# Performance work log

Hardware: AMD Instinct MI355X
Metric: run time of the kernel (lower is better)

The kernel has to match this reference:

```python
import jax, jax.numpy as jnp
import numpy as np

N_NODES = 100000
N_IN = 256
N_OUT = 64
N_EDGES = 1600000


def setup_inputs() -> dict:
    key = jax.random.key(0)
    k_x, k_w, k_b, k_v, k_r, k_c = jax.random.split(key, 6)
    x = jax.random.normal(k_x, (N_NODES, N_IN), dtype=jnp.float32)
    W = jax.random.normal(k_w, (N_IN, N_OUT), dtype=jnp.float32) * (1.0 / np.sqrt(N_IN))
    b = jax.random.normal(k_b, (N_OUT,), dtype=jnp.float32) * 0.01
    adj_vals = jax.random.uniform(k_v, (N_EDGES,), dtype=jnp.float32)
    edge_rows = jax.random.randint(k_r, (N_EDGES,), 0, N_NODES, dtype=jnp.int32)
    edge_cols = jax.random.randint(k_c, (N_EDGES,), 0, N_NODES, dtype=jnp.int32)
    return {"x": x, "W": W, "b": b, "adj_vals": adj_vals,
            "edge_rows": edge_rows, "edge_cols": edge_cols}


def reference(x, W, b, adj_vals, edge_rows, edge_cols):
    # linear projection: [N, n_in] @ [n_in, n_out] + b -> [N, n_out]
    h = x @ W + b
    # sparse-dense matmul: out[i] = sum_e adj_vals[e] * h[edge_cols[e]] for edge_rows[e]==i
    msgs = h[edge_cols] * adj_vals[:, None]  # [E, n_out]
    out = jax.ops.segment_sum(msgs, edge_rows, num_segments=N_NODES)
    return out
```

## Files before the change

kernel.cpp:

```cpp
#include <hip/hip_runtime.h>


#include <stdint.h>

constexpr int KDIM = 256;
constexpr int MOUT = 64;

constexpr int RPB = 128;
constexpr int RPB_SHIFT = 7;
constexpr int MAXBUCK = 1024;
constexpr int CHUNK = 2048;
constexpr int COL_BITS = 20;
constexpr int COL_MASK = (1 << COL_BITS) - 1;
constexpr int SORT_CAP = 4096;
constexpr int HIST_BLOCKS = 256;
constexpr int GROWS = 64;

typedef __attribute__((ext_vector_type(8))) short short8v;
typedef __attribute__((ext_vector_type(4))) float f32x4;

__device__ __forceinline__ unsigned short f2bf(float f) {
  unsigned u = __float_as_uint(f);
  return (unsigned short)((u + 0x7fffu + ((u >> 16) & 1u)) >> 16);
}

__device__ __forceinline__ void async_ld16(const float* g, float* l) {
  __builtin_amdgcn_global_load_lds(
      (const __attribute__((address_space(1))) void*)g,
      (__attribute__((address_space(3))) void*)l, 16, 0, 0);
}

__global__ __launch_bounds__(256)
void prep(const float* __restrict__ W, unsigned short* __restrict__ wt,
          const int* __restrict__ rows, int* __restrict__ bcnt, int E, int nbuck) {
  const int t = threadIdx.x;
  if ((int)blockIdx.x < 64) {
    int n = blockIdx.x;
    wt[n * KDIM + t] = f2bf(W[(size_t)t * MOUT + n]);
    return;
  }
  __shared__ int cnt[MAXBUCK];
  for (int i = t; i < nbuck; i += 256) cnt[i] = 0;
  __syncthreads();
  const int b0 = blockIdx.x - 64;
  for (int e = b0 * 256 + t; e < E; e += HIST_BLOCKS * 256)
    atomicAdd(&cnt[rows[e] >> RPB_SHIFT], 1);
  __syncthreads();
  for (int i = t; i < nbuck; i += 256)
    if (cnt[i]) atomicAdd(&bcnt[i], cnt[i]);
}

__global__ __launch_bounds__(1024)
void scan_buckets(const int* __restrict__ bcnt, int* __restrict__ bptr,
                  int* __restrict__ bcur, int nbuck, int E) {
  __shared__ int buf[1024];
  __shared__ int carry;
  const int t = threadIdx.x;
  if (t == 0) carry = 0;
  __syncthreads();
  for (int c0 = 0; c0 < nbuck; c0 += 1024) {
    int i = c0 + t;
    int x = (i < nbuck) ? bcnt[i] : 0;
    buf[t] = x;
    __syncthreads();
    for (int off = 1; off < 1024; off <<= 1) {
      int v = (t >= off) ? buf[t - off] : 0;
      __syncthreads();
      buf[t] += v;
      __syncthreads();
    }
    int incl = buf[t];
    int base = carry;
    if (i < nbuck) {
      int ex = base + incl - x;
      bptr[i] = ex;
      bcur[i] = ex;
    }
    __syncthreads();
    if (t == 1023) carry = base + incl;
    __syncthreads();
  }
  if (t == 0) bptr[nbuck] = E;
}

__global__ __launch_bounds__(256, 4)
void gemm_scatter(const float* __restrict__ x, const unsigned short* __restrict__ wt,
                  const float* __restrict__ bvec, unsigned short* __restrict__ h,
                  const int* __restrict__ rows, const int* __restrict__ cols,
                  const float* __restrict__ vals, int* __restrict__ bcur,
                  int2* __restrict__ sorted, int gemmBlocks, int N, int E, int nbuck) {
  __shared__ __align__(16) char smem[16384];
  const int t = threadIdx.x;

  if ((int)blockIdx.x < gemmBlocks) {
    auto xs = reinterpret_cast<float(*)[GROWS][32]>(smem);
    const int wave = t >> 6, lane = t & 63;
    const int lo = lane & 15, hi = lane >> 4;
    const int row0 = blockIdx.x * GROWS;
    const int rowbase = row0 + wave * 16;

    auto stage = [&](int kt, int b) {
#pragma unroll
      for (int i = 0; i < 2; ++i) {
        int g = i * 256 + t;
        int row = g >> 3, c = g & 7;
        int csw = c ^ (row & 7);
        int rr = row0 + row; if (rr >= N) rr = N - 1;
        const float* src = &x[(size_t)rr * KDIM + kt * 32 + csw * 4];
        float* dst = &xs[b][0][0] + (size_t)(i * 256 + (t & 192)) * 4;
        async_ld16(src, dst);
      }
    };

    float bias[4];
#pragma unroll
    for (int nt = 0; nt < 4; ++nt) bias[nt] = bvec[nt * 16 + lo];

    const int lr = wave * 16 + lo;
    const int go0 = (((hi * 2)    ) ^ (lr & 7)) * 4;
    const int go1 = (((hi * 2) + 1) ^ (lr & 7)) * 4;

    f32x4 acc[4] = {};
    short8v wfr[2][4];
#pragma unroll
    for (int nt = 0; nt < 4; ++nt)
      wfr[0][nt] = *reinterpret_cast<const short8v*>(&wt[(size_t)(nt * 16 + lo) * KDIM + hi * 8]);
    stage(0, 0);

#pragma unroll
    for (int kt = 0; kt < 8; ++kt) {
      const int cb = kt & 1;
      __syncthreads();
      if (kt < 7) {
        stage(kt + 1, cb ^ 1);
#pragma unroll
        for (int nt = 0; nt < 4; ++nt)
          wfr[cb ^ 1][nt] = *reinterpret_cast<const short8v*>(
              &wt[(size_t)(nt * 16 + lo) * KDIM + (kt + 1) * 32 + hi * 8]);
      }
      float4 p0 = *reinterpret_cast<const float4*>(&xs[cb][lr][go0]);
      float4 p1 = *reinterpret_cast<const float4*>(&xs[cb][lr][go1]);
      short8v a;
      a[0] = (short)f2bf(p0.x); a[1] = (short)f2bf(p0.y);
      a[2] = (short)f2bf(p0.z); a[3] = (short)f2bf(p0.w);
      a[4] = (short)f2bf(p1.x); a[5] = (short)f2bf(p1.y);
      a[6] = (short)f2bf(p1.z); a[7] = (short)f2bf(p1.w);
#pragma unroll
      for (int nt = 0; nt < 4; ++nt)
        acc[nt] = __builtin_amdgcn_mfma_f32_16x16x32_bf16(a, wfr[cb][nt], acc[nt], 0, 0, 0);
    }

#pragma unroll
    for (int reg = 0; reg < 4; ++reg) {
      int row = rowbase + hi * 4 + reg;
      if (row < N) {
#pragma unroll
        for (int nt = 0; nt < 4; ++nt)
          h[(size_t)row * MOUT + nt * 16 + lo] = f2bf(acc[nt][reg] + bias[nt]);
      }
    }
    return;
  }

  int* lcnt  = reinterpret_cast<int*>(smem);
  int* lbase = lcnt + MAXBUCK;
  const int cid = blockIdx.x - gemmBlocks;
  const int e0 = cid * CHUNK;
  const int e1 = min(e0 + CHUNK, E);

  for (int i = t; i < nbuck; i += 256) lcnt[i] = 0;
  __syncthreads();
  for (int e = e0 + t; e < e1; e += 256)
    atomicAdd(&lcnt[rows[e] >> RPB_SHIFT], 1);
  __syncthreads();
  for (int i = t; i < nbuck; i += 256) {
    int c = lcnt[i];
    lbase[i] = c ? atomicAdd(&bcur[i], c) : 0;
  }
  __syncthreads();
  for (int i = t; i < nbuck; i += 256) lcnt[i] = 0;
  __syncthreads();
  for (int e = e0 + t; e < e1; e += 256) {
    int r = rows[e];
    int b = r >> RPB_SHIFT;
    int lrow = r & (RPB - 1);
    int pos = lbase[b] + atomicAdd(&lcnt[b], 1);
    sorted[pos] = make_int2((lrow << COL_BITS) | cols[e], __float_as_int(vals[e]));
  }
}

__global__ __launch_bounds__(256)
void bucket_sort(int2* __restrict__ sorted, const int* __restrict__ bptr,
                 int* __restrict__ row_ptr, int* __restrict__ bflag,
                 int N, int E, int nbuck) {
  __shared__ int2 eds[SORT_CAP];
  __shared__ int lcnt[RPB];
  __shared__ int loff[RPB];
  __shared__ int lcur[RPB];
  const int t = threadIdx.x;
  const int b = blockIdx.x;
  const int s = bptr[b];
  const int e = bptr[b + 1];
  const int cnt = e - s;
  const int row0 = b << RPB_SHIFT;

  if (b == 0 && t == 0) row_ptr[N] = E;

  if (cnt > SORT_CAP) {
    if (t == 0) bflag[b] = 1;
    if (t < RPB && row0 + t < N) row_ptr[row0 + t] = s;
    return;
  }
  if (t == 0) bflag[b] = 0;

  if (t < RPB) lcnt[t] = 0;
  __syncthreads();
  for (int j = s + t; j < e; j += 256) {
    int2 p = sorted[j];
    eds[j - s] = p;
    atomicAdd(&lcnt[p.x >> COL_BITS], 1);
  }
  __syncthreads();
  if (t < RPB) loff[t] = lcnt[t];
  __syncthreads();
  for (int off = 1; off < RPB; off <<= 1) {
    int v = (t < RPB && t >= off) ? loff[t - off] : 0;
    __syncthreads();
    if (t < RPB) loff[t] += v;
    __syncthreads();
  }
  if (t < RPB) {
    int ex = loff[t] - lcnt[t];
    loff[t] = ex;
    lcur[t] = 0;
    int grow = row0 + t;
    if (grow < N) row_ptr[grow] = s + ex;
  }
  __syncthreads();
  for (int idx = t; idx < cnt; idx += 256) {
    int2 p = eds[idx];
    int lr = p.x >> COL_BITS;
    int pos = s + loff[lr] + atomicAdd(&lcur[lr], 1);
    sorted[pos] = p;
  }
}

__device__ __forceinline__ void edge_fma(float* acc, const unsigned short* h,
                                         int2 p, int part) {
  float v = __int_as_float(p.y);
  int col = p.x & COL_MASK;
  uint4 hv = *reinterpret_cast<const uint4*>(&h[(size_t)col * MOUT + part * 8]);
  acc[0] += v * __uint_as_float(hv.x << 16);
  acc[1] += v * __uint_as_float(hv.x & 0xffff0000u);
  acc[2] += v * __uint_as_float(hv.y << 16);
  acc[3] += v * __uint_as_float(hv.y & 0xffff0000u);
  acc[4] += v * __uint_as_float(hv.z << 16);
  acc[5] += v * __uint_as_float(hv.z & 0xffff0000u);
  acc[6] += v * __uint_as_float(hv.w << 16);
  acc[7] += v * __uint_as_float(hv.w & 0xffff0000u);
}

__global__ __launch_bounds__(256)
void reduce_rows(const unsigned short* __restrict__ h, const int2* __restrict__ sorted,
                 const int* __restrict__ row_ptr, const int* __restrict__ bptr,
                 const int* __restrict__ bflag, float* __restrict__ out, int N) {
  int row = (blockIdx.x * 256 + threadIdx.x) >> 6;
  if (row >= N) return;
  int lane = threadIdx.x & 63;
  int slot = lane >> 3;
  int part = lane & 7;
  int b = row >> RPB_SHIFT;
  int lrow = row & (RPB - 1);
  bool filt = bflag[b] != 0;

  float acc[8];
#pragma unroll
  for (int i = 0; i < 8; ++i) acc[i] = 0.f;

  if (!filt) {
    int s = row_ptr[row];
    int e = row_ptr[row + 1];
    int j = s + slot;
    for (; j + 8 < e; j += 16) {
      int2 p0 = sorted[j];
      int2 p1 = sorted[j + 8];
      float v0 = __int_as_float(p0.y);
      float v1 = __int_as_float(p1.y);
      uint4 h0 = *reinterpret_cast<const uint4*>(
          &h[(size_t)(p0.x & COL_MASK) * MOUT + part * 8]);
      uint4 h1 = *reinterpret_cast<const uint4*>(
          &h[(size_t)(p1.x & COL_MASK) * MOUT + part * 8]);
      acc[0] += v0 * __uint_as_float(h0.x << 16);
      acc[1] += v0 * __uint_as_float(h0.x & 0xffff0000u);
      acc[2] += v0 * __uint_as_float(h0.y << 16);
      acc[3] += v0 * __uint_as_float(h0.y & 0xffff0000u);
      acc[4] += v0 * __uint_as_float(h0.z << 16);
      acc[5] += v0 * __uint_as_float(h0.z & 0xffff0000u);
      acc[6] += v0 * __uint_as_float(h0.w << 16);
      acc[7] += v0 * __uint_as_float(h0.w & 0xffff0000u);
      acc[0] += v1 * __uint_as_float(h1.x << 16);
      acc[1] += v1 * __uint_as_float(h1.x & 0xffff0000u);
      acc[2] += v1 * __uint_as_float(h1.y << 16);
      acc[3] += v1 * __uint_as_float(h1.y & 0xffff0000u);
      acc[4] += v1 * __uint_as_float(h1.z << 16);
      acc[5] += v1 * __uint_as_float(h1.z & 0xffff0000u);
      acc[6] += v1 * __uint_as_float(h1.w << 16);
      acc[7] += v1 * __uint_as_float(h1.w & 0xffff0000u);
    }
    if (j < e) edge_fma(acc, h, sorted[j], part);
  } else {
    int s = bptr[b];
    int e = bptr[b + 1];
    for (int j = s + slot; j < e; j += 8) {
      int2 p = sorted[j];
      if ((p.x >> COL_BITS) != lrow) continue;
      edge_fma(acc, h, p, part);
    }
  }

#pragma unroll
  for (int m = 8; m <= 32; m <<= 1)
#pragma unroll
    for (int i = 0; i < 8; ++i)
      acc[i] += __shfl_xor(acc[i], m, 64);

  if (slot == 0) {
    float* op = &out[(size_t)row * MOUT + part * 8];
    *reinterpret_cast<float4*>(op)     = make_float4(acc[0], acc[1], acc[2], acc[3]);
    *reinterpret_cast<float4*>(op + 4) = make_float4(acc[4], acc[5], acc[6], acc[7]);
  }
}

__global__ __launch_bounds__(256)
void scatter_edges(const unsigned short* __restrict__ h, const float* __restrict__ vals,
                   const int* __restrict__ rows, const int* __restrict__ cols,
                   float* __restrict__ out, int E) {
  long long idx = (long long)blockIdx.x * blockDim.x + threadIdx.x;
  int e = (int)(idx >> 4);
  int part = (int)(idx & 15);
  if (e >= E) return;
  int r = rows[e];
  int c = cols[e];
  float v = vals[e];
  uint2 hv = *reinterpret_cast<const uint2*>(&h[(size_t)c * MOUT + part * 4]);
  float* op = &out[(size_t)r * MOUT + part * 4];
  atomicAdd(op + 0, v * __uint_as_float(hv.x << 16));
  atomicAdd(op + 1, v * __uint_as_float(hv.x & 0xffff0000u));
  atomicAdd(op + 2, v * __uint_as_float(hv.y << 16));
  atomicAdd(op + 3, v * __uint_as_float(hv.y & 0xffff0000u));
}

__global__ __launch_bounds__(256)
void wt_transpose(const float* __restrict__ W, unsigned short* __restrict__ wt) {
  int n = blockIdx.x;
  int k = threadIdx.x;
  wt[n * KDIM + k] = f2bf(W[(size_t)k * MOUT + n]);
}

static inline size_t align256(size_t x) { return (x + 255) & ~(size_t)255; }

extern "C" void kernel_launch(void* const* d_in, const int* in_sizes, int n_in,
                              void* d_out, int out_size, void* d_ws, size_t ws_size,
                              hipStream_t stream) {
  const float* x    = (const float*)d_in[0];
  const float* W    = (const float*)d_in[1];
  const float* bvec = (const float*)d_in[2];
  const float* vals = (const float*)d_in[3];
  const int* erows  = (const int*)d_in[4];
  const int* ecols  = (const int*)d_in[5];
  float* out = (float*)d_out;

  const int N = in_sizes[0] / KDIM;
  const int E = in_sizes[3];
  const int nbuck = (N + RPB - 1) / RPB;

  char* ws = (char*)d_ws;
  size_t off_h  = 0;
  size_t off_wt = align256(off_h + (size_t)N * MOUT * sizeof(short));
  size_t off_bp = align256(off_wt + (size_t)MOUT * KDIM * sizeof(short));
  size_t off_bc = align256(off_bp + (size_t)(nbuck + 1) * sizeof(int));
  size_t off_cu = align256(off_bc + (size_t)nbuck * sizeof(int));
  size_t off_bf = align256(off_cu + (size_t)nbuck * sizeof(int));
  size_t off_rp = align256(off_bf + (size_t)nbuck * sizeof(int));
  size_t off_sp = align256(off_rp + (size_t)(N + 1) * sizeof(int));
  size_t need   = off_sp + (size_t)E * sizeof(int2);

  unsigned short* h  = (unsigned short*)(ws + off_h);
  unsigned short* wt = (unsigned short*)(ws + off_wt);

  dim3 blk256(256);
  const int gemmBlocks = (N + GROWS - 1) / GROWS;

  if (ws_size >= need && nbuck <= MAXBUCK && N < (1 << COL_BITS)) {
    int* bptr  = (int*)(ws + off_bp);
    int* bcnt  = (int*)(ws + off_bc);
    int* bcur  = (int*)(ws + off_cu);
    int* bflag = (int*)(ws + off_bf);
    int* row_ptr = (int*)(ws + off_rp);
    int2* sorted = (int2*)(ws + off_sp);

    hipMemsetAsync(bcnt, 0, (size_t)nbuck * sizeof(int), stream);
    prep<<<dim3(64 + HIST_BLOCKS), blk256, 0, stream>>>(W, wt, erows, bcnt, E, nbuck);
    scan_buckets<<<dim3(1), dim3(1024), 0, stream>>>(bcnt, bptr, bcur, nbuck, E);
    const int scatBlocks = (E + CHUNK - 1) / CHUNK;
    gemm_scatter<<<dim3(gemmBlocks + scatBlocks), blk256, 0, stream>>>(
        x, wt, bvec, h, erows, ecols, vals, bcur, sorted, gemmBlocks, N, E, nbuck);
    bucket_sort<<<dim3(nbuck), blk256, 0, stream>>>(sorted, bptr, row_ptr, bflag, N, E, nbuck);
    reduce_rows<<<dim3(((size_t)N * 64 + 255) / 256), blk256, 0, stream>>>(
        h, sorted, row_ptr, bptr, bflag, out, N);
  } else {
    wt_transpose<<<dim3(MOUT), blk256, 0, stream>>>(W, wt);
    gemm_scatter<<<dim3(gemmBlocks), blk256, 0, stream>>>(
        x, wt, bvec, h, erows, ecols, vals, (int*)wt, (int2*)h, gemmBlocks, N, E, nbuck);
    hipMemsetAsync(d_out, 0, (size_t)out_size * sizeof(float), stream);
    long long work = (long long)E * 16;
    scatter_edges<<<dim3((unsigned)((work + 255) / 256)), blk256, 0, stream>>>(h, vals, erows, ecols, out, E);
  }
}
```

Baseline: 139.3 us.

## Split fused GEMM/scatter kernel and deepen GEMM K-tile to 64

Measured after the change: 144.5 us. 1.04x slower.

```diff
diff --git a/kernel.cpp b/kernel.cpp
--- a/kernel.cpp
+++ b/kernel.cpp
@@ -9,7 +9,7 @@
 constexpr int RPB = 128;
 constexpr int RPB_SHIFT = 7;
 constexpr int MAXBUCK = 1024;
-constexpr int CHUNK = 2048;
+constexpr int CHUNK = 4096;
 constexpr int COL_BITS = 20;
 constexpr int COL_MASK = (1 << COL_BITS) - 1;
 constexpr int SORT_CAP = 4096;
@@ -84,62 +84,62 @@
 }
 
 __global__ __launch_bounds__(256, 4)
-void gemm_scatter(const float* __restrict__ x, const unsigned short* __restrict__ wt,
-                  const float* __restrict__ bvec, unsigned short* __restrict__ h,
-                  const int* __restrict__ rows, const int* __restrict__ cols,
-                  const float* __restrict__ vals, int* __restrict__ bcur,
-                  int2* __restrict__ sorted, int gemmBlocks, int N, int E, int nbuck) {
-  __shared__ __align__(16) char smem[16384];
+void gemm_mfma(const float* __restrict__ x, const unsigned short* __restrict__ wt,
+               const float* __restrict__ bvec, unsigned short* __restrict__ h, int N) {
+  __shared__ __align__(16) float xs[2][GROWS][64];
   const int t = threadIdx.x;
-
-  if ((int)blockIdx.x < gemmBlocks) {
-    auto xs = reinterpret_cast<float(*)[GROWS][32]>(smem);
-    const int wave = t >> 6, lane = t & 63;
-    const int lo = lane & 15, hi = lane >> 4;
-    const int row0 = blockIdx.x * GROWS;
-    const int rowbase = row0 + wave * 16;
-
-    auto stage = [&](int kt, int b) {
-#pragma unroll
-      for (int i = 0; i < 2; ++i) {
-        int g = i * 256 + t;
-        int row = g >> 3, c = g & 7;
-        int csw = c ^ (row & 7);
-        int rr = row0 + row; if (rr >= N) rr = N - 1;
-        const float* src = &x[(size_t)rr * KDIM + kt * 32 + csw * 4];
-        float* dst = &xs[b][0][0] + (size_t)(i * 256 + (t & 192)) * 4;
-        async_ld16(src, dst);
-      }
-    };
-
-    float bias[4];
-#pragma unroll
-    for (int nt = 0; nt < 4; ++nt) bias[nt] = bvec[nt * 16 + lo];
-
-    const int lr = wave * 16 + lo;
-    const int go0 = (((hi * 2)    ) ^ (lr & 7)) * 4;
-    const int go1 = (((hi * 2) + 1) ^ (lr & 7)) * 4;
-
-    f32x4 acc[4] = {};
-    short8v wfr[2][4];
+  const int wave = t >> 6, lane = t & 63;
+  const int lo = lane & 15, hi = lane >> 4;
+  const int row0 = blockIdx.x * GROWS;
+  const int rowbase = row0 + wave * 16;
+
+  auto stage = [&](int kt, int b) {
+#pragma unroll
+    for (int i = 0; i < 4; ++i) {
+      int g = i * 256 + t;
+      int row = g >> 4, c = g & 15;
+      int csw = c ^ (row & 15);
+      int rr = row0 + row; if (rr >= N) rr = N - 1;
+      const float* src = &x[(size_t)rr * KDIM + kt * 64 + csw * 4];
+      float* dst = &xs[b][0][0] + (size_t)(i * 256 + (t & 192)) * 4;
+      async_ld16(src, dst);
+    }
+  };
+
+  float bias[4];
+#pragma unroll
+  for (int nt = 0; nt < 4; ++nt) bias[nt] = bvec[nt * 16 + lo];
+
+  const int lr = wave * 16 + lo;
+  f32x4 acc[4] = {};
+  short8v wfr[2][2][4];
+#pragma unroll
+  for (int ks = 0; ks < 2; ++ks)
 #pragma unroll
     for (int nt = 0; nt < 4; ++nt)
-      wfr[0][nt] = *reinterpret_cast<const short8v*>(&wt[(size_t)(nt * 16 + lo) * KDIM + hi * 8]);
-    stage(0, 0);
-
-#pragma unroll
-    for (int kt = 0; kt < 8; ++kt) {
-      const int cb = kt & 1;
-      __syncthreads();
-      if (kt < 7) {
-        stage(kt + 1, cb ^ 1);
+      wfr[0][ks][nt] = *reinterpret_cast<const short8v*>(
+          &wt[(size_t)(nt * 16 + lo) * KDIM + ks * 32 + hi * 8]);
+  stage(0, 0);
+
+#pragma unroll
+  for (int kt = 0; kt < 4; ++kt) {
+    const int cb = kt & 1;
+    __syncthreads();
+    if (kt < 3) {
+      stage(kt + 1, cb ^ 1);
+#pragma unroll
+      for (int ks = 0; ks < 2; ++ks)
 #pragma unroll
         for (int nt = 0; nt < 4; ++nt)
-          wfr[cb ^ 1][nt] = *reinterpret_cast<const short8v*>(
-              &wt[(size_t)(nt * 16 + lo) * KDIM + (kt + 1) * 32 + hi * 8]);
-      }
-      float4 p0 = *reinterpret_cast<const float4*>(&xs[cb][lr][go0]);
-      float4 p1 = *reinterpret_cast<const float4*>(&xs[cb][lr][go1]);
+          wfr[cb ^ 1][ks][nt] = *reinterpret_cast<const short8v*>(
+              &wt[(size_t)(nt * 16 + lo) * KDIM + (kt + 1) * 64 + ks * 32 + hi * 8]);
+    }
+#pragma unroll
+    for (int ks = 0; ks < 2; ++ks) {
+      int c0 = ((ks * 8 + hi * 2)     ^ (lr & 15)) * 4;
+      int c1 = ((ks * 8 + hi * 2 + 1) ^ (lr & 15)) * 4;
+      float4 p0 = *reinterpret_cast<const float4*>(&xs[cb][lr][c0]);
+      float4 p1 = *reinterpret_cast<const float4*>(&xs[cb][lr][c1]);
       short8v a;
       a[0] = (short)f2bf(p0.x); a[1] = (short)f2bf(p0.y);
       a[2] = (short)f2bf(p0.z); a[3] = (short)f2bf(p0.w);
@@ -147,25 +147,29 @@
       a[6] = (short)f2bf(p1.z); a[7] = (short)f2bf(p1.w);
 #pragma unroll
       for (int nt = 0; nt < 4; ++nt)
-        acc[nt] = __builtin_amdgcn_mfma_f32_16x16x32_bf16(a, wfr[cb][nt], acc[nt], 0, 0, 0);
-    }
-
-#pragma unroll
-    for (int reg = 0; reg < 4; ++reg) {
-      int row = rowbase + hi * 4 + reg;
-      if (row < N) {
-#pragma unroll
-        for (int nt = 0; nt < 4; ++nt)
-          h[(size_t)row * MOUT + nt * 16 + lo] = f2bf(acc[nt][reg] + bias[nt]);
-      }
-    }
-    return;
-  }
-
-  int* lcnt  = reinterpret_cast<int*>(smem);
-  int* lbase = lcnt + MAXBUCK;
-  const int cid = blockIdx.x - gemmBlocks;
-  const int e0 = cid * CHUNK;
+        acc[nt] = __builtin_amdgcn_mfma_f32_16x16x32_bf16(a, wfr[cb][ks][nt], acc[nt], 0, 0, 0);
+    }
+  }
+
+#pragma unroll
+  for (int reg = 0; reg < 4; ++reg) {
+    int row = rowbase + hi * 4 + reg;
+    if (row < N) {
+#pragma unroll
+      for (int nt = 0; nt < 4; ++nt)
+        h[(size_t)row * MOUT + nt * 16 + lo] = f2bf(acc[nt][reg] + bias[nt]);
+    }
+  }
+}
+
+__global__ __launch_bounds__(256)
+void edge_scatter(const int* __restrict__ rows, const int* __restrict__ cols,
+                  const float* __restrict__ vals, int* __restrict__ bcur,
+                  int2* __restrict__ sorted, int E, int nbuck) {
+  __shared__ int lcnt[MAXBUCK];
+  __shared__ int lbase[MAXBUCK];
+  const int t = threadIdx.x;
+  const int e0 = blockIdx.x * CHUNK;
   const int e1 = min(e0 + CHUNK, E);
 
   for (int i = t; i < nbuck; i += 256) lcnt[i] = 0;
@@ -402,16 +406,15 @@
     hipMemsetAsync(bcnt, 0, (size_t)nbuck * sizeof(int), stream);
     prep<<<dim3(64 + HIST_BLOCKS), blk256, 0, stream>>>(W, wt, erows, bcnt, E, nbuck);
     scan_buckets<<<dim3(1), dim3(1024), 0, stream>>>(bcnt, bptr, bcur, nbuck, E);
-    const int scatBlocks = (E + CHUNK - 1) / CHUNK;
-    gemm_scatter<<<dim3(gemmBlocks + scatBlocks), blk256, 0, stream>>>(
-        x, wt, bvec, h, erows, ecols, vals, bcur, sorted, gemmBlocks, N, E, nbuck);
+    gemm_mfma<<<dim3(gemmBlocks), blk256, 0, stream>>>(x, wt, bvec, h, N);
+    edge_scatter<<<dim3((E + CHUNK - 1) / CHUNK), blk256, 0, stream>>>(
+        erows, ecols, vals, bcur, sorted, E, nbuck);
     bucket_sort<<<dim3(nbuck), blk256, 0, stream>>>(sorted, bptr, row_ptr, bflag, N, E, nbuck);
     reduce_rows<<<dim3(((size_t)N * 64 + 255) / 256), blk256, 0, stream>>>(
         h, sorted, row_ptr, bptr, bflag, out, N);
   } else {
     wt_transpose<<<dim3(MOUT), blk256, 0, stream>>>(W, wt);
-    gemm_scatter<<<dim3(gemmBlocks), blk256, 0, stream>>>(
-        x, wt, bvec, h, erows, ecols, vals, (int*)wt, (int2*)h, gemmBlocks, N, E, nbuck);
+    gemm_mfma<<<dim3(gemmBlocks), blk256, 0, stream>>>(x, wt, bvec, h, N);
     hipMemsetAsync(d_out, 0, (size_t)out_size * sizeof(float), stream);
     long long work = (long long)E * 16;
     scatter_edges<<<dim3((unsigned)((work + 255) / 256)), blk256, 0, stream>>>(h, vals, erows, ecols, out, E);
```
